# Kernel tuning notes

Hardware: AMD Instinct MI355X
Metric: run time of the kernel (lower is better)

Reference implementation:

```python
import jax, jax.numpy as jnp
import numpy as np

N, E, R, L = 20000, 160000, 3, 2
IN, HID, H, OUT = 64, 128, 16, 1
FH = HID // H   # per-head dim = 8
HD2 = HID // 2  # MLP bottleneck = 64


def setup_inputs() -> dict:
    key = jax.random.key(0)
    ks = iter(jax.random.split(key, 40))
    def w(*shape):
        return jax.random.normal(next(ks), shape, jnp.float32) * 0.05
    inp = dict(
        inputs=jax.random.normal(next(ks), (N, IN), jnp.float32),
        src=jax.random.randint(next(ks), (R, E), 0, N, dtype=jnp.int32),
        dst=jax.random.randint(next(ks), (R, E), 0, N, dtype=jnp.int32),
        e1_W=w(IN, HID), e1_b=jnp.zeros(HID), e_g=jnp.ones(HID), e_bt=jnp.zeros(HID),
        e2_W=w(HID, HID), e2_b=jnp.zeros(HID),
        gat_W=w(L, R, HID, HID), gat_al=w(L, R, H, FH), gat_ar=w(L, R, H, FH),
        gat_b=jnp.zeros((L, R, HID)),
        attn_p=w(L, R, HID),
        m1_W=w(L, HID, HD2), m1_b=jnp.zeros((L, HD2)), m_g=jnp.ones((L, HD2)), m_bt=jnp.zeros((L, HD2)),
        m2_W=w(L, HD2, HID), m2_b=jnp.zeros((L, HID)),
        d1_W=w(HID, HD2), d1_b=jnp.zeros(HD2), d_g=jnp.ones(HD2), d_bt=jnp.zeros(HD2),
        d2_W=w(HD2, OUT), d2_b=jnp.zeros(OUT),
    )
    return inp


def _bn(x, g, b):
    # BatchNorm1d, training mode: biased batch statistics, eps=1e-5
    mu = x.mean(0)
    var = jnp.mean((x - mu) ** 2, 0)
    return g * (x - mu) * jax.lax.rsqrt(var + 1e-5) + b


def _mlp(x, W1, b1, g, bt, W2, b2, skip=False):
    h = jax.nn.relu(_bn(x @ W1 + b1, g, bt))
    o = h @ W2 + b2
    return o + h if skip else o


def _gat(x, W, al, ar, b, src, dst):
    # single-relation DGL GATConv (feat_drop=attn_drop=0, neg_slope=0.2, bias)
    z = (x @ W).reshape(N, H, FH)                 # [N,H,FH]
    el = (z * al).sum(-1)                          # [N,H]
    er = (z * ar).sum(-1)                          # [N,H]
    e = jax.nn.leaky_relu(el[src] + er[dst], 0.2)  # [E,H]
    m = jax.ops.segment_max(e, dst, num_segments=N)
    m = jnp.where(jnp.isfinite(m), m, 0.0)
    ex = jnp.exp(e - m[dst])
    s = jax.ops.segment_sum(ex, dst, num_segments=N)
    alpha = ex / s[dst]                            # edge softmax over in-edges
    out = jax.ops.segment_sum(alpha[:, :, None] * z[src], dst, num_segments=N)
    return out.reshape(N, HID) + b                 # flatten heads + bias


def reference(inputs, src, dst, e1_W, e1_b, e_g, e_bt, e2_W, e2_b,
              gat_W, gat_al, gat_ar, gat_b, attn_p,
              m1_W, m1_b, m_g, m_bt, m2_W, m2_b,
              d1_W, d1_b, d_g, d_bt, d2_W, d2_b):
    h = _mlp(inputs, e1_W, e1_b, e_g, e_bt, e2_W, e2_b, skip=True)  # embed, skip
    gat_v = jax.vmap(_gat, in_axes=(None, 0, 0, 0, 0, 0, 0))        # over relations
    for l in range(L):
        stacked = gat_v(h, gat_W[l], gat_al[l], gat_ar[l], gat_b[l], src, dst)  # [R,N,HID]
        w = jax.nn.softmax(attn_p[l], axis=0)        # per-dim softmax over relations [R,HID]
        v = jnp.einsum('rnf,rf->nf', stacked, w)     # attn-weighted relation agg
        h = _mlp(v, m1_W[l], m1_b[l], m_g[l], m_bt[l], m2_W[l], m2_b[l]) + h
    return _mlp(h, d1_W, d1_b, d_g, d_bt, d2_W, d2_b)
```

## Files before the change

kernel.cpp:

```cpp
#include <hip/hip_runtime.h>
#include <math.h>

constexpr int kN   = 20000;
constexpr int kE   = 160000;
constexpr int kR   = 3;
constexpr int kL   = 2;
constexpr int kIN  = 64;
constexpr int kHID = 128;
constexpr int kH   = 16;
constexpr int kFH  = 8;
constexpr int kHD2 = 64;
constexpr int kSB  = (kN + 255) / 256;

typedef __bf16 bf16x8 __attribute__((ext_vector_type(8)));
typedef float  f32x4  __attribute__((ext_vector_type(4)));

__device__ __forceinline__ bf16x8 ldfrag(const __bf16* p) {
  return __builtin_bit_cast(bf16x8, *(const uint4*)p);
}
__device__ __forceinline__ f32x4 MF(bf16x8 a, bf16x8 b, f32x4 c) {
  return __builtin_amdgcn_mfma_f32_16x16x32_bf16(a, b, c, 0, 0, 0);
}

__device__ __forceinline__ void splitrow(const float* __restrict__ rowbase, int koff,
                                         bool bn, const float* scS, const float* shS,
                                         bf16x8& hi, bf16x8& lo) {
  float4 xa = *(const float4*)(rowbase + koff);
  float4 xb = *(const float4*)(rowbase + koff + 4);
  float x[8] = {xa.x, xa.y, xa.z, xa.w, xb.x, xb.y, xb.z, xb.w};
  union { __bf16 b[8]; bf16x8 v; } uh, ul;
#pragma unroll
  for (int e = 0; e < 8; e++) {
    float y = x[e];
    if (bn) y = fmaxf(fmaf(y, scS[koff + e], shS[koff + e]), 0.f);
    __bf16 hb = (__bf16)y;
    uh.b[e] = hb;
    ul.b[e] = (__bf16)(y - (float)hb);
  }
  hi = uh.v; lo = ul.v;
}

__global__ __launch_bounds__(256) void mgemm_kernel(
    const float* __restrict__ A, const __bf16* __restrict__ WT,
    const float* __restrict__ bias, const float* __restrict__ resf, int resmode,
    const float* __restrict__ bnstat, const float* __restrict__ bng,
    const float* __restrict__ bnbt, float invn,
    float* __restrict__ statS,
    float* __restrict__ Cf, __bf16* __restrict__ Chi,
    const float* __restrict__ alb, const float* __restrict__ arb,
    float* __restrict__ elout,
    int n, int k, int m, long wstride, long cstride) {
  __shared__ __bf16 Bh[64][136];
  __shared__ __bf16 Bl[64][136];
  __shared__ float scS[128], shS[128];
  const int t  = threadIdx.x;
  const int w  = t >> 6;
  const int l  = t & 63;
  const int lr = l & 15;
  const int lg = l >> 4;
  const int rb = blockIdx.x * 128 + w * 32;
  const int c0 = blockIdx.y * 64;
  const __bf16* Whi = WT + (size_t)blockIdx.z * wstride;
  const __bf16* Wlo = Whi + (size_t)k * m;
  if (Chi) Chi += (size_t)blockIdx.z * cstride;
  const float* al = alb ? alb + blockIdx.z * kHID : nullptr;
  const float* ar = arb ? arb + blockIdx.z * kHID : nullptr;
  float* elo = elout ? elout + blockIdx.z * 32 : nullptr;

  const bool bn = bnstat != nullptr;
  if (bn && t < k) {
    float mu  = bnstat[t] * invn;
    float var = bnstat[k + t] * invn - mu * mu;
    float s = bng[t] * rsqrtf(var + 1e-5f);
    scS[t] = s; shS[t] = bnbt[t] - mu * s;
  }
  const int kseg = k >> 3;
  for (int idx = t; idx < 64 * kseg; idx += 256) {
    int col = idx / kseg, seg = idx - col * kseg;
    *(uint4*)&Bh[col][seg * 8] = *(const uint4*)&Whi[(size_t)(c0 + col) * k + seg * 8];
    *(uint4*)&Bl[col][seg * 8] = *(const uint4*)&Wlo[(size_t)(c0 + col) * k + seg * 8];
  }
  __syncthreads();

  int r0 = rb + lr;      if (r0 > n - 1) r0 = n - 1;
  int r1 = rb + 16 + lr; if (r1 > n - 1) r1 = n - 1;
  f32x4 acc[2][4] = {};

  for (int ks = 0; ks < (k >> 5); ks++) {
    const int koff = ks * 32 + lg * 8;
    bf16x8 a0h, a0l, a1h, a1l;
    splitrow(&A[(size_t)r0 * k], koff, bn, scS, shS, a0h, a0l);
    splitrow(&A[(size_t)r1 * k], koff, bn, scS, shS, a1h, a1l);
#pragma unroll
    for (int j = 0; j < 4; j++) {
      bf16x8 bh = ldfrag(&Bh[j * 16 + lr][koff]);
      bf16x8 bl = ldfrag(&Bl[j * 16 + lr][koff]);
      acc[0][j] = MF(a0h, bh, acc[0][j]);
      acc[0][j] = MF(a0l, bh, acc[0][j]);
      acc[0][j] = MF(a0h, bl, acc[0][j]);
      acc[1][j] = MF(a1h, bh, acc[1][j]);
      acc[1][j] = MF(a1l, bh, acc[1][j]);
      acc[1][j] = MF(a1h, bl, acc[1][j]);
    }
  }

  float s[4] = {}, s2[4] = {};
#pragma unroll
  for (int i = 0; i < 2; i++) {
#pragma unroll
    for (int q = 0; q < 4; q++) {
      int row = rb + i * 16 + lg * 4 + q;
      bool ok = row < n;
#pragma unroll
      for (int j = 0; j < 4; j++) {
        int col = c0 + j * 16 + lr;
        float v = acc[i][j][q];
        if (bias) v += bias[col];
        size_t off = (size_t)row * m + col;
        if (ok) {
          if (resmode == 1) v += resf[off];
          else if (resmode == 2) v += fmaxf(fmaf(resf[off], scS[col], shS[col]), 0.f);
          if (Cf) Cf[off] = v;
          if (Chi) Chi[off] = (__bf16)v;
          s[j] += v; s2[j] += v * v;
        }
      }
    }
  }
  if (statS) {
    __syncthreads();
    float* red = (float*)&Bh[0][0];
#pragma unroll
    for (int j = 0; j < 4; j++) {
      float a = s[j], b = s2[j];
      a += __shfl_xor(a, 16, 64); a += __shfl_xor(a, 32, 64);
      b += __shfl_xor(b, 16, 64); b += __shfl_xor(b, 32, 64);
      if (lg == 0) { red[w * 64 + j * 16 + lr] = a; red[256 + w * 64 + j * 16 + lr] = b; }
    }
    __syncthreads();
    if (t < 64) {
      float a = red[t] + red[64 + t] + red[128 + t] + red[192 + t];
      float b = red[256 + t] + red[320 + t] + red[384 + t] + red[448 + t];
      atomicAdd(&statS[c0 + t], a);
      atomicAdd(&statS[m + c0 + t], b);
    }
  }
  if (al) {
#pragma unroll
    for (int i = 0; i < 2; i++) {
#pragma unroll
      for (int q = 0; q < 4; q++) {
        int row = rb + i * 16 + lg * 4 + q;
#pragma unroll
        for (int j = 0; j < 4; j++) {
          int col = c0 + j * 16 + lr;
          float zv = acc[i][j][q];
          float pl = zv * al[col];
          float pr = zv * ar[col];
          pl += __shfl_xor(pl, 1, 64); pl += __shfl_xor(pl, 2, 64); pl += __shfl_xor(pl, 4, 64);
          pr += __shfl_xor(pr, 1, 64); pr += __shfl_xor(pr, 2, 64); pr += __shfl_xor(pr, 4, 64);
          if ((lr & 7) == 0 && row < n) {
            int hd = col >> 3;
            elo[(size_t)row * kHID + hd * 2]     = pl;
            elo[(size_t)row * kHID + hd * 2 + 1] = pr;
          }
        }
      }
    }
  }
}

struct WDesc { const float* src; long doff; int k, m; };
struct WDescs { WDesc d[13]; };
__global__ void wprep_kernel(WDescs ds, __bf16* __restrict__ wt) {
  WDesc dd = ds.d[blockIdx.y];
  int idx = blockIdx.x * 256 + threadIdx.x;
  if (idx >= dd.k * dd.m) return;
  int row = idx / dd.m, col = idx - row * dd.m;
  float v = dd.src[idx];
  __bf16 hb = (__bf16)v;
  __bf16 lb = (__bf16)(v - (float)hb);
  wt[dd.doff + (size_t)col * dd.k + row] = hb;
  wt[dd.doff + (size_t)dd.k * dd.m + (size_t)col * dd.k + row] = lb;
}

__global__ void hist_kernel(const int* __restrict__ dst, int* __restrict__ deg) {
  int r = blockIdx.y;
  int e = blockIdx.x * 256 + threadIdx.x;
  if (e < kE) atomicAdd(&deg[r * kN + dst[r * kE + e]], 1);
}

__global__ void bsum_kernel(const int* __restrict__ deg, int* __restrict__ bsum) {
  int r = blockIdx.y;
  int j = blockIdx.x * 256 + threadIdx.x;
  int x = (j < kN) ? deg[r * kN + j] : 0;
  __shared__ int shm[256];
  shm[threadIdx.x] = x;
  __syncthreads();
  for (int off = 128; off > 0; off >>= 1) {
    if (threadIdx.x < off) shm[threadIdx.x] += shm[threadIdx.x + off];
    __syncthreads();
  }
  if (threadIdx.x == 0) bsum[r * kSB + blockIdx.x] = shm[0];
}

__global__ void bscan_kernel(int* __restrict__ bsum) {
  __shared__ int shm[kR * kSB];
  int t = threadIdx.x;
  for (int i = t; i < kR * kSB; i += 256) shm[i] = bsum[i];
  __syncthreads();
  if (t < kR) {
    int run = 0;
    for (int b = 0; b < kSB; b++) { int v = shm[t * kSB + b]; shm[t * kSB + b] = run; run += v; }
  }
  __syncthreads();
  for (int i = t; i < kR * kSB; i += 256) bsum[i] = shm[i];
}

__global__ void scan2_kernel(const int* __restrict__ deg, const int* __restrict__ bsum,
                             int* __restrict__ rowptr) {
  int r = blockIdx.y;
  int t = threadIdx.x;
  int j = blockIdx.x * 256 + t;
  int x = (j < kN) ? deg[r * kN + j] : 0;
  int lane = t & 63, w = t >> 6;
  int v = x;
  for (int off = 1; off < 64; off <<= 1) {
    int y = __shfl_up(v, off, 64);
    if (lane >= off) v += y;
  }
  __shared__ int wtot[4];
  if (lane == 63) wtot[w] = v;
  __syncthreads();
  int add = bsum[r * kSB + blockIdx.x];
  for (int i = 0; i < 4; i++) if (i < w) add += wtot[i];
  if (j < kN) rowptr[r * (kN + 1) + j] = add + v - x;
  if (blockIdx.x == 0 && t == 0) rowptr[r * (kN + 1) + kN] = kE;
}

__global__ void scatter_kernel(const int* __restrict__ src, const int* __restrict__ dst,
                               const int* __restrict__ rowptr, int* __restrict__ cursor,
                               int* __restrict__ col) {
  int r = blockIdx.y;
  int e = blockIdx.x * 256 + threadIdx.x;
  if (e < kE) {
    int d = dst[r * kE + e];
    int p = atomicAdd(&cursor[r * kN + d], 1);
    col[r * kE + rowptr[r * (kN + 1) + d] + p] = src[r * kE + e];
  }
}

__global__ void gat3_kernel(const int* __restrict__ rowptr, const int* __restrict__ colidx,
                            const ushort* __restrict__ z, const float* __restrict__ elr,
                            const float* __restrict__ attn_pl, const float* __restrict__ gat_bl,
                            float* __restrict__ vv) {
  __shared__ float wsmS[kR * kHID], cvecS[kHID];
  int t = threadIdx.x;
  if (t < kHID) {
    float p0 = attn_pl[t], p1 = attn_pl[kHID + t], p2 = attn_pl[2 * kHID + t];
    float mx = fmaxf(p0, fmaxf(p1, p2));
    float e0 = __expf(p0 - mx), e1 = __expf(p1 - mx), e2 = __expf(p2 - mx);
    float si = 1.f / (e0 + e1 + e2);
    wsmS[t] = e0 * si; wsmS[kHID + t] = e1 * si; wsmS[2 * kHID + t] = e2 * si;
    cvecS[t] = (e0 * gat_bl[t] + e1 * gat_bl[kHID + t] + e2 * gat_bl[2 * kHID + t]) * si;
  }
  __syncthreads();
  int idx = blockIdx.x * 256 + t;
  if (idx >= kN * kH) return;
  int d = idx >> 4, hh = idx & 15;
  float out[kFH];
#pragma unroll
  for (int f = 0; f < kFH; f++) out[f] = cvecS[(hh << 3) + f];
  for (int r = 0; r < kR; r++) {
    const int* rp = rowptr + r * (kN + 1);
    const int* ci = colidx + (size_t)r * kE;
    const ushort* zr = z + (size_t)r * kN * kHID;
    float erd = elr[((size_t)d << 7) + r * 32 + (hh << 1) + 1];
    int beg = rp[d], end = rp[d + 1];
    float s = 0.f;
    float acc[kFH] = {};
    for (int p = beg; p < end; p++) {
      int sv = ci[p];
      float v = elr[((size_t)sv << 7) + r * 32 + (hh << 1)] + erd;
      v = v > 0.f ? v : 0.2f * v;
      float ex = __expf(v);
      s += ex;
      uint4 zz = *(const uint4*)(zr + ((size_t)sv << 7) + (hh << 3));
      acc[0] = fmaf(ex, __uint_as_float(zz.x << 16),         acc[0]);
      acc[1] = fmaf(ex, __uint_as_float(zz.x & 0xffff0000u), acc[1]);
      acc[2] = fmaf(ex, __uint_as_float(zz.y << 16),         acc[2]);
      acc[3] = fmaf(ex, __uint_as_float(zz.y & 0xffff0000u), acc[3]);
      acc[4] = fmaf(ex, __uint_as_float(zz.z << 16),         acc[4]);
      acc[5] = fmaf(ex, __uint_as_float(zz.z & 0xffff0000u), acc[5]);
      acc[6] = fmaf(ex, __uint_as_float(zz.w << 16),         acc[6]);
      acc[7] = fmaf(ex, __uint_as_float(zz.w & 0xffff0000u), acc[7]);
    }
    float inv = s > 0.f ? 1.f / s : 0.f;
    const float* wp = wsmS + r * kHID + (hh << 3);
#pragma unroll
    for (int f = 0; f < kFH; f++) out[f] = fmaf(wp[f] * inv, acc[f], out[f]);
  }
  float4* vp = (float4*)(vv + ((size_t)d << 7) + (hh << 3));
  vp[0] = make_float4(out[0], out[1], out[2], out[3]);
  vp[1] = make_float4(out[4], out[5], out[6], out[7]);
}

__global__ void gemv_out_kernel(const float* __restrict__ A, const float* __restrict__ statS,
                                const float* __restrict__ g, const float* __restrict__ bt,
                                float invn, const float* __restrict__ w,
                                const float* __restrict__ b, float* __restrict__ out,
                                int n, int k) {
  __shared__ float scS[kHD2], shS[kHD2];
  int t = threadIdx.x;
  if (t < k) {
    float mu  = statS[t] * invn;
    float var = statS[k + t] * invn - mu * mu;
    float s = g[t] * rsqrtf(var + 1e-5f);
    scS[t] = s; shS[t] = bt[t] - mu * s;
  }
  __syncthreads();
  int i = blockIdx.x * 256 + t;
  if (i >= n) return;
  const float4* a = (const float4*)(A + (size_t)i * k);
  float acc = b[0];
  for (int j4 = 0; j4 < k / 4; j4++) {
    float4 x = a[j4];
    int c = j4 * 4;
    acc = fmaf(fmaxf(fmaf(x.x, scS[c],     shS[c]),     0.f), w[c],     acc);
    acc = fmaf(fmaxf(fmaf(x.y, scS[c + 1], shS[c + 1]), 0.f), w[c + 1], acc);
    acc = fmaf(fmaxf(fmaf(x.z, scS[c + 2], shS[c + 2]), 0.f), w[c + 2], acc);
    acc = fmaf(fmaxf(fmaf(x.w, scS[c + 3], shS[c + 3]), 0.f), w[c + 3], acc);
  }
  out[i] = acc;
}

extern "C" void kernel_launch(void* const* d_in, const int* in_sizes, int n_in,
                              void* d_out, int out_size, void* d_ws, size_t ws_size,
                              hipStream_t stream) {
  const float* inputs = (const float*)d_in[0];
  const int*   src    = (const int*)d_in[1];
  const int*   dst    = (const int*)d_in[2];
  const float* e1_W   = (const float*)d_in[3];
  const float* e1_b   = (const float*)d_in[4];
  const float* e_g    = (const float*)d_in[5];
  const float* e_bt   = (const float*)d_in[6];
  const float* e2_W   = (const float*)d_in[7];
  const float* e2_b   = (const float*)d_in[8];
  const float* gat_W  = (const float*)d_in[9];
  const float* gat_al = (const float*)d_in[10];
  const float* gat_ar = (const float*)d_in[11];
  const float* gat_b  = (const float*)d_in[12];
  const float* attn_p = (const float*)d_in[13];
  const float* m1_W   = (const float*)d_in[14];
  const float* m1_b   = (const float*)d_in[15];
  const float* m_g    = (const float*)d_in[16];
  const float* m_bt   = (const float*)d_in[17];
  const float* m2_W   = (const float*)d_in[18];
  const float* m2_b   = (const float*)d_in[19];
  const float* d1_W   = (const float*)d_in[20];
  const float* d1_b   = (const float*)d_in[21];
  const float* d_g    = (const float*)d_in[22];
  const float* d_bt   = (const float*)d_in[23];
  const float* d2_W   = (const float*)d_in[24];
  const float* d2_b   = (const float*)d_in[25];

  float* ws = (float*)d_ws;
  size_t o = 0;
  float*  h     = ws + o; o += (size_t)kN * kHID;
  float*  bufA  = ws + o; o += (size_t)kN * kHID;
  float*  elr   = ws + o; o += (size_t)kN * kHID;
  float*  vv    = ws + o; o += (size_t)kN * kHID;
  __bf16* z     = (__bf16*)(ws + o); o += (size_t)kR * kN * kHID / 2;
  __bf16* wt    = (__bf16*)(ws + o); o += 327680 / 2;
  float*  stats = ws + o; o += 640;
  int* rowptr   = (int*)(ws + o); o += (size_t)kR * (kN + 1);
  int* colidx   = (int*)(ws + o); o += (size_t)kR * kE;
  int* degcur   = (int*)(ws + o); o += (size_t)6 * kN;
  int* bsum     = (int*)(ws + o); o += kR * kSB;
  (void)ws_size; (void)in_sizes; (void)n_in; (void)out_size;

  int* deg    = degcur;
  int* cursor = degcur + 3 * kN;
  float* stat_e1 = stats;
  float* stat_m1[2] = {stats + 256, stats + 384};
  float* stat_d1 = stats + 512;

  const long kWE1 = 0, kWE2 = 16384, kWZ = 49152;
  const long kWM1_0 = 245760, kWM1_1 = 262144, kWM2_0 = 278528, kWM2_1 = 294912, kWD1 = 311296;

  auto nb = [](long t) { return (int)((t + 255) / 256); };
  const long NHh = (long)kN * kH;
  const dim3 gE(nb(kE), kR);
  const dim3 gS(kSB, kR);
  const dim3 gM128((kN + 127) / 128, 2, 1);
  const dim3 gM64((kN + 127) / 128, 1, 1);
  const dim3 gMZ((kN + 127) / 128, 2, kR);
  const float invn = 1.0f / kN;
  float* F0 = nullptr; const float* cF0 = nullptr;

  hipMemsetAsync(degcur, 0, (size_t)6 * kN * sizeof(int), stream);
  hist_kernel<<<gE, 256, 0, stream>>>(dst, deg);
  bsum_kernel<<<gS, 256, 0, stream>>>(deg, bsum);
  bscan_kernel<<<1, 256, 0, stream>>>(bsum);
  scan2_kernel<<<gS, 256, 0, stream>>>(deg, bsum, rowptr);
  scatter_kernel<<<gE, 256, 0, stream>>>(src, dst, rowptr, cursor, colidx);

  WDescs wd;
  wd.d[0] = {e1_W, kWE1, kIN, kHID};
  wd.d[1] = {e2_W, kWE2, kHID, kHID};
  for (int i = 0; i < 6; i++) wd.d[2 + i] = {gat_W + (size_t)i * 16384, kWZ + (long)i * 32768, kHID, kHID};
  wd.d[8]  = {m1_W,        kWM1_0, kHID, kHD2};
  wd.d[9]  = {m1_W + 8192, kWM1_1, kHID, kHD2};
  wd.d[10] = {m2_W,        kWM2_0, kHD2, kHID};
  wd.d[11] = {m2_W + 8192, kWM2_1, kHD2, kHID};
  wd.d[12] = {d1_W,        kWD1,   kHID, kHD2};
  wprep_kernel<<<dim3(64, 13), 256, 0, stream>>>(wd, wt);
  hipMemsetAsync(stats, 0, 640 * sizeof(float), stream);

  mgemm_kernel<<<gM128, 256, 0, stream>>>(inputs, wt + kWE1, e1_b, cF0, 0,
                                          cF0, cF0, cF0, invn, stat_e1, bufA, nullptr,
                                          cF0, cF0, F0, kN, kIN, kHID, 0, 0);
  mgemm_kernel<<<gM128, 256, 0, stream>>>(bufA, wt + kWE2, e2_b, bufA, 2,
                                          stat_e1, e_g, e_bt, invn, F0, h, nullptr,
                                          cF0, cF0, F0, kN, kHID, kHID, 0, 0);

  for (int l = 0; l < kL; l++) {
    mgemm_kernel<<<gMZ, 256, 0, stream>>>(h, wt + kWZ + (long)l * 3 * 32768, cF0, cF0, 0,
                                          cF0, cF0, cF0, invn, F0, F0, z,
                                          gat_al + (size_t)l * kR * kHID,
                                          gat_ar + (size_t)l * kR * kHID, elr,
                                          kN, kHID, kHID, 32768, (long)kN * kHID);
    gat3_kernel<<<nb(NHh), 256, 0, stream>>>(rowptr, colidx, (const ushort*)z, elr,
                                             attn_p + (size_t)l * kR * kHID,
                                             gat_b + (size_t)l * kR * kHID, vv);
    mgemm_kernel<<<gM64, 256, 0, stream>>>(vv, wt + (l ? kWM1_1 : kWM1_0),
                                           m1_b + (size_t)l * kHD2, cF0, 0,
                                           cF0, cF0, cF0, invn, stat_m1[l], bufA, nullptr,
                                           cF0, cF0, F0, kN, kHID, kHD2, 0, 0);
    mgemm_kernel<<<gM128, 256, 0, stream>>>(bufA, wt + (l ? kWM2_1 : kWM2_0),
                                            m2_b + (size_t)l * kHID, h, 1,
                                            stat_m1[l], m_g + (size_t)l * kHD2,
                                            m_bt + (size_t)l * kHD2, invn, F0, h, nullptr,
                                            cF0, cF0, F0, kN, kHD2, kHID, 0, 0);
  }

  mgemm_kernel<<<gM64, 256, 0, stream>>>(h, wt + kWD1, d1_b, cF0, 0,
                                         cF0, cF0, cF0, invn, stat_d1, bufA, nullptr,
                                         cF0, cF0, F0, kN, kHID, kHD2, 0, 0);
  gemv_out_kernel<<<nb(kN), 256, 0, stream>>>(bufA, stat_d1, d_g, d_bt, invn,
                                              d2_W, d2_b, (float*)d_out, kN, kHD2);
}
```

Measured before the change: 331.6 us.

## Single-kernel CSR scan, split GAT head into halves, merge memsets

Replaces the three-kernel block-sum/scan/scan2 rowptr construction with a single 1024-thread block per relation that does a chunked serial-plus-warp scan. It also splits each GAT (node, head) work item across two threads handling 4 features each, doubling parallelism and halving per-thread register accumulators. Stats are moved next to degcur so one memset clears both. The cost is that each thread redundantly recomputes the edge softmax terms, and the scan now runs in only three blocks.

After: 371.6 us. 1.12x slower.

```diff
diff --git a/kernel.cpp b/kernel.cpp
--- a/kernel.cpp
+++ b/kernel.cpp
@@ -10,7 +10,6 @@
 constexpr int kH   = 16;
 constexpr int kFH  = 8;
 constexpr int kHD2 = 64;
-constexpr int kSB  = (kN + 255) / 256;
 
 typedef __bf16 bf16x8 __attribute__((ext_vector_type(8)));
 typedef float  f32x4  __attribute__((ext_vector_type(4)));
@@ -190,52 +189,39 @@
   if (e < kE) atomicAdd(&deg[r * kN + dst[r * kE + e]], 1);
 }
 
-__global__ void bsum_kernel(const int* __restrict__ deg, int* __restrict__ bsum) {
-  int r = blockIdx.y;
-  int j = blockIdx.x * 256 + threadIdx.x;
-  int x = (j < kN) ? deg[r * kN + j] : 0;
-  __shared__ int shm[256];
-  shm[threadIdx.x] = x;
-  __syncthreads();
-  for (int off = 128; off > 0; off >>= 1) {
-    if (threadIdx.x < off) shm[threadIdx.x] += shm[threadIdx.x + off];
-    __syncthreads();
-  }
-  if (threadIdx.x == 0) bsum[r * kSB + blockIdx.x] = shm[0];
-}
-
-__global__ void bscan_kernel(int* __restrict__ bsum) {
-  __shared__ int shm[kR * kSB];
-  int t = threadIdx.x;
-  for (int i = t; i < kR * kSB; i += 256) shm[i] = bsum[i];
-  __syncthreads();
-  if (t < kR) {
-    int run = 0;
-    for (int b = 0; b < kSB; b++) { int v = shm[t * kSB + b]; shm[t * kSB + b] = run; run += v; }
-  }
-  __syncthreads();
-  for (int i = t; i < kR * kSB; i += 256) bsum[i] = shm[i];
-}
-
-__global__ void scan2_kernel(const int* __restrict__ deg, const int* __restrict__ bsum,
-                             int* __restrict__ rowptr) {
-  int r = blockIdx.y;
-  int t = threadIdx.x;
-  int j = blockIdx.x * 256 + t;
-  int x = (j < kN) ? deg[r * kN + j] : 0;
-  int lane = t & 63, w = t >> 6;
-  int v = x;
+__global__ __launch_bounds__(1024) void csr_scan_kernel(const int* __restrict__ deg,
+                                                        int* __restrict__ rowptr) {
+  const int r = blockIdx.y;
+  const int* dg = deg + r * kN;
+  int* rp = rowptr + r * (kN + 1);
+  const int t = threadIdx.x;
+  constexpr int C = (kN + 1023) / 1024;
+  const int base = t * C;
+  int sum = 0;
+#pragma unroll
+  for (int i = 0; i < C; i++) {
+    int j = base + i;
+    if (j < kN) sum += dg[j];
+  }
+  __shared__ int warpTot[16];
+  int lane = t & 63, wid = t >> 6;
+  int v = sum;
   for (int off = 1; off < 64; off <<= 1) {
     int y = __shfl_up(v, off, 64);
     if (lane >= off) v += y;
   }
-  __shared__ int wtot[4];
-  if (lane == 63) wtot[w] = v;
+  if (lane == 63) warpTot[wid] = v;
   __syncthreads();
-  int add = bsum[r * kSB + blockIdx.x];
-  for (int i = 0; i < 4; i++) if (i < w) add += wtot[i];
-  if (j < kN) rowptr[r * (kN + 1) + j] = add + v - x;
-  if (blockIdx.x == 0 && t == 0) rowptr[r * (kN + 1) + kN] = kE;
+  int wadd = 0;
+#pragma unroll
+  for (int i = 0; i < 16; i++) if (i < wid) wadd += warpTot[i];
+  int run = wadd + v - sum;
+#pragma unroll
+  for (int i = 0; i < C; i++) {
+    int j = base + i;
+    if (j < kN) { rp[j] = run; run += dg[j]; }
+  }
+  if (t == 1023) rp[kN] = run;
 }
 
 __global__ void scatter_kernel(const int* __restrict__ src, const int* __restrict__ dst,
@@ -266,11 +252,14 @@
   }
   __syncthreads();
   int idx = blockIdx.x * 256 + t;
-  if (idx >= kN * kH) return;
-  int d = idx >> 4, hh = idx & 15;
-  float out[kFH];
-#pragma unroll
-  for (int f = 0; f < kFH; f++) out[f] = cvecS[(hh << 3) + f];
+  if (idx >= kN * kH * 2) return;
+  int half = idx & 1;
+  int hh   = (idx >> 1) & 15;
+  int d    = idx >> 5;
+  int fo   = (hh << 3) + (half << 2);
+  float out[4];
+#pragma unroll
+  for (int f = 0; f < 4; f++) out[f] = cvecS[fo + f];
   for (int r = 0; r < kR; r++) {
     const int* rp = rowptr + r * (kN + 1);
     const int* ci = colidx + (size_t)r * kE;
@@ -278,31 +267,25 @@
     float erd = elr[((size_t)d << 7) + r * 32 + (hh << 1) + 1];
     int beg = rp[d], end = rp[d + 1];
     float s = 0.f;
-    float acc[kFH] = {};
+    float acc[4] = {};
     for (int p = beg; p < end; p++) {
       int sv = ci[p];
       float v = elr[((size_t)sv << 7) + r * 32 + (hh << 1)] + erd;
       v = v > 0.f ? v : 0.2f * v;
       float ex = __expf(v);
       s += ex;
-      uint4 zz = *(const uint4*)(zr + ((size_t)sv << 7) + (hh << 3));
+      uint2 zz = *(const uint2*)(zr + ((size_t)sv << 7) + fo);
       acc[0] = fmaf(ex, __uint_as_float(zz.x << 16),         acc[0]);
       acc[1] = fmaf(ex, __uint_as_float(zz.x & 0xffff0000u), acc[1]);
       acc[2] = fmaf(ex, __uint_as_float(zz.y << 16),         acc[2]);
       acc[3] = fmaf(ex, __uint_as_float(zz.y & 0xffff0000u), acc[3]);
-      acc[4] = fmaf(ex, __uint_as_float(zz.z << 16),         acc[4]);
-      acc[5] = fmaf(ex, __uint_as_float(zz.z & 0xffff0000u), acc[5]);
-      acc[6] = fmaf(ex, __uint_as_float(zz.w << 16),         acc[6]);
-      acc[7] = fmaf(ex, __uint_as_float(zz.w & 0xffff0000u), acc[7]);
     }
     float inv = s > 0.f ? 1.f / s : 0.f;
-    const float* wp = wsmS + r * kHID + (hh << 3);
-#pragma unroll
-    for (int f = 0; f < kFH; f++) out[f] = fmaf(wp[f] * inv, acc[f], out[f]);
-  }
-  float4* vp = (float4*)(vv + ((size_t)d << 7) + (hh << 3));
-  vp[0] = make_float4(out[0], out[1], out[2], out[3]);
-  vp[1] = make_float4(out[4], out[5], out[6], out[7]);
+    const float* wp = wsmS + r * kHID + fo;
+#pragma unroll
+    for (int f = 0; f < 4; f++) out[f] = fmaf(wp[f] * inv, acc[f], out[f]);
+  }
+  *(float4*)(vv + ((size_t)d << 7) + fo) = make_float4(out[0], out[1], out[2], out[3]);
 }
 
 __global__ void gemv_out_kernel(const float* __restrict__ A, const float* __restrict__ statS,
@@ -372,11 +355,10 @@
   float*  vv    = ws + o; o += (size_t)kN * kHID;
   __bf16* z     = (__bf16*)(ws + o); o += (size_t)kR * kN * kHID / 2;
   __bf16* wt    = (__bf16*)(ws + o); o += 327680 / 2;
-  float*  stats = ws + o; o += 640;
+  int* degcur   = (int*)(ws + o); o += (size_t)6 * kN;
+  float* stats  = ws + o; o += 640;
   int* rowptr   = (int*)(ws + o); o += (size_t)kR * (kN + 1);
   int* colidx   = (int*)(ws + o); o += (size_t)kR * kE;
-  int* degcur   = (int*)(ws + o); o += (size_t)6 * kN;
-  int* bsum     = (int*)(ws + o); o += kR * kSB;
   (void)ws_size; (void)in_sizes; (void)n_in; (void)out_size;
 
   int* deg    = degcur;
@@ -389,20 +371,16 @@
   const long kWM1_0 = 245760, kWM1_1 = 262144, kWM2_0 = 278528, kWM2_1 = 294912, kWD1 = 311296;
 
   auto nb = [](long t) { return (int)((t + 255) / 256); };
-  const long NHh = (long)kN * kH;
   const dim3 gE(nb(kE), kR);
-  const dim3 gS(kSB, kR);
   const dim3 gM128((kN + 127) / 128, 2, 1);
   const dim3 gM64((kN + 127) / 128, 1, 1);
   const dim3 gMZ((kN + 127) / 128, 2, kR);
   const float invn = 1.0f / kN;
   float* F0 = nullptr; const float* cF0 = nullptr;
 
-  hipMemsetAsync(degcur, 0, (size_t)6 * kN * sizeof(int), stream);
+  hipMemsetAsync(degcur, 0, ((size_t)6 * kN + 640) * sizeof(int), stream);
   hist_kernel<<<gE, 256, 0, stream>>>(dst, deg);
-  bsum_kernel<<<gS, 256, 0, stream>>>(deg, bsum);
-  bscan_kernel<<<1, 256, 0, stream>>>(bsum);
-  scan2_kernel<<<gS, 256, 0, stream>>>(deg, bsum, rowptr);
+  csr_scan_kernel<<<dim3(1, kR), 1024, 0, stream>>>(deg, rowptr);
   scatter_kernel<<<gE, 256, 0, stream>>>(src, dst, rowptr, cursor, colidx);
 
   WDescs wd;
@@ -415,7 +393,6 @@
   wd.d[11] = {m2_W + 8192, kWM2_1, kHD2, kHID};
   wd.d[12] = {d1_W,        kWD1,   kHID, kHD2};
   wprep_kernel<<<dim3(64, 13), 256, 0, stream>>>(wd, wt);
-  hipMemsetAsync(stats, 0, 640 * sizeof(float), stream);
 
   mgemm_kernel<<<gM128, 256, 0, stream>>>(inputs, wt + kWE1, e1_b, cF0, 0,
                                           cF0, cF0, cF0, invn, stat_e1, bufA, nullptr,
@@ -430,7 +407,7 @@
                                           gat_al + (size_t)l * kR * kHID,
                                           gat_ar + (size_t)l * kR * kHID, elr,
                                           kN, kHID, kHID, 32768, (long)kN * kHID);
-    gat3_kernel<<<nb(NHh), 256, 0, stream>>>(rowptr, colidx, (const ushort*)z, elr,
+    gat3_kernel<<<nb((long)kN * kH * 2), 256, 0, stream>>>(rowptr, colidx, (const ushort*)z, elr,
                                              attn_p + (size_t)l * kR * kHID,
                                              gat_b + (size_t)l * kR * kHID, vv);
     mgemm_kernel<<<gM64, 256, 0, stream>>>(vv, wt + (l ? kWM1_1 : kWM1_0),
```
